# Optimization experiments

Hardware: AMD Instinct MI355X
Metric: run time of the kernel (lower is better)

The kernel has to match this reference:

```python
import jax, jax.numpy as jnp
import numpy as np

E = 16        # n_routed_experts
K = 2         # n_activated_experts (top-k)
DIM = 1024    # model dim
INTER = 704   # moe_inter_dim
B, S = 4, 1024


def setup_inputs() -> dict:
    key = jax.random.key(0)
    ks = jax.random.split(key, 5)
    x = jax.random.normal(ks[0], (B, S, DIM), dtype=jnp.float32)
    Wg = jax.random.normal(ks[1], (E, DIM), dtype=jnp.float32) * 0.02   # gate (Linear, no bias)
    W1 = jax.random.normal(ks[2], (E, DIM, INTER), dtype=jnp.float32) * 0.02
    W3 = jax.random.normal(ks[3], (E, DIM, INTER), dtype=jnp.float32) * 0.02
    W2 = jax.random.normal(ks[4], (E, INTER, DIM), dtype=jnp.float32) * 0.02
    return {"x": x, "Wg": Wg, "W1": W1, "W2": W2, "W3": W3}


def reference(x, Wg, W1, W2, W3):
    # Single-process semantics of MoEWithAll2All: the all2all dispatch/combine is
    # pure communication; the math is: softmax router -> top-k -> renormalize ->
    # per-expert SwiGLU MLP on routed tokens -> weighted combine at original slots.
    Bb, Ss, D = x.shape
    xf = x.reshape(-1, D)                              # [N, D], N = B*S
    logits = xf @ Wg.T                                 # [N, E]
    probs = jax.nn.softmax(logits, axis=-1)
    topw, topi = jax.lax.top_k(probs, K)               # [N, K]
    topw = topw / topw.sum(axis=-1, keepdims=True)
    # gates[n, e] = routed weight of token n for expert e (0 if not routed):
    # identical math to the masked gather/scatter dispatch in the original.
    gates = (jax.nn.one_hot(topi, E, dtype=xf.dtype) * topw[..., None]).sum(axis=1)  # [N, E]
    out = jnp.zeros_like(xf)
    for e in range(E):                                 # small fixed loop over experts
        h = jax.nn.silu(xf @ W1[e]) * (xf @ W3[e])     # SwiGLU expert, [N, INTER]
        out = out + gates[:, e:e + 1] * (h @ W2[e])    # combine with gate weights
    return out.reshape(Bb, Ss, D)
```

## Files before the change

### kernel.cpp

```cpp
#include <hip/hip_runtime.h>

#define NTOK 4096
#define DDIM 1024
#define IDIM 704
#define NEXP 16
#define NSLOT 8192
#define MAXT 128
#define NPAD1 768

typedef __attribute__((ext_vector_type(8))) short bf16x8;
typedef __attribute__((ext_vector_type(4))) float f32x4;
typedef __attribute__((ext_vector_type(4))) unsigned short us4;
typedef __attribute__((ext_vector_type(8))) unsigned short us8;

__device__ __forceinline__ unsigned short f2bf(float f) {
  union { float f; unsigned int u; } v; v.f = f;
  unsigned int r = v.u + 0x7fffu + ((v.u >> 16) & 1u);
  return (unsigned short)(r >> 16);
}

__device__ __forceinline__ void gload_lds16(const void* g, void* l) {
  __builtin_amdgcn_global_load_lds((const __attribute__((address_space(1))) void*)g,
                                   (__attribute__((address_space(3))) void*)l, 16, 0, 0);
}

__global__ void k_router(const float* __restrict__ x, const float* __restrict__ Wg,
                         int* __restrict__ tok_e, float* __restrict__ tok_w,
                         unsigned short* __restrict__ Xb) {
  int lane = threadIdx.x & 63;
  int wv = threadIdx.x >> 6;
  int t = blockIdx.x * 4 + wv;
  const f32x4* xr = (const f32x4*)(x + (size_t)t * DDIM);
  us4* xbr = (us4*)(Xb + (size_t)t * DDIM);
  f32x4 xv[4];
#pragma unroll
  for (int c = 0; c < 4; ++c) {
    xv[c] = xr[c * 64 + lane];
    us4 o;
#pragma unroll
    for (int j = 0; j < 4; ++j) o[j] = f2bf(xv[c][j]);
    xbr[c * 64 + lane] = o;
  }
  float p[NEXP];
#pragma unroll
  for (int e = 0; e < NEXP; ++e) {
    const f32x4* wr = (const f32x4*)(Wg + (size_t)e * DDIM);
    float s = 0.f;
#pragma unroll
    for (int c = 0; c < 4; ++c) {
      f32x4 w4 = wr[c * 64 + lane];
      s += xv[c][0]*w4[0] + xv[c][1]*w4[1] + xv[c][2]*w4[2] + xv[c][3]*w4[3];
    }
    p[e] = s;
  }
#pragma unroll
  for (int off = 32; off >= 1; off >>= 1) {
#pragma unroll
    for (int e = 0; e < NEXP; ++e) p[e] += __shfl_xor(p[e], off);
  }
  int i0 = 0; float b0 = p[0];
#pragma unroll
  for (int e = 1; e < NEXP; ++e) if (p[e] > b0) { b0 = p[e]; i0 = e; }
  int i1 = -1; float b1 = -3.4e38f;
#pragma unroll
  for (int e = 0; e < NEXP; ++e) if (e != i0 && p[e] > b1) { b1 = p[e]; i1 = e; }
  if (lane == 0) {
    float w0 = 1.f / (1.f + __expf(b1 - b0));
    tok_e[2*t] = i0; tok_e[2*t+1] = i1;
    tok_w[2*t] = w0; tok_w[2*t+1] = 1.f - w0;
  }
}

__global__ void k_wtrans(const float* __restrict__ src, unsigned short* __restrict__ dst,
                         int ksz, int nsz, int npad) {
  int e = blockIdx.z;
  int k0 = blockIdx.x * 64, n0 = blockIdx.y * 64;
  src += (size_t)e * ksz * nsz;
  dst += (size_t)e * npad * ksz;
  int t = threadIdx.x;
  if (n0 >= nsz) {
    int nr = t >> 3, kc0 = (t & 7) * 8;
    us8 z = (us8)(unsigned short)0;
#pragma unroll
    for (int p = 0; p < 2; ++p)
      *(us8*)(dst + (size_t)(n0 + nr + p * 32) * ksz + k0 + kc0) = z;
    return;
  }
  __shared__ unsigned short lds[64 * 64];
  int kr4 = (t >> 4) * 4, nc4 = (t & 15) * 4;
  f32x4 v[4];
#pragma unroll
  for (int j = 0; j < 4; ++j)
    v[j] = *(const f32x4*)(src + (size_t)(k0 + kr4 + j) * nsz + n0 + nc4);
  int c8 = kr4 >> 3, half = (kr4 >> 2) & 1;
#pragma unroll
  for (int i = 0; i < 4; ++i) {
    us4 o;
#pragma unroll
    for (int j = 0; j < 4; ++j) o[j] = f2bf(v[j][i]);
    int row = nc4 + i;
    int addr = row * 64 + ((c8 ^ ((row >> 2) & 7)) << 3) + half * 4;
    *(us4*)(lds + addr) = o;
  }
  __syncthreads();
  int nr = t >> 3, kc8 = t & 7;
#pragma unroll
  for (int p = 0; p < 2; ++p) {
    int row = nr + p * 32;
    us8 o = *(const us8*)(lds + row * 64 + ((kc8 ^ ((row >> 2) & 7)) << 3));
    *(us8*)(dst + (size_t)(n0 + row) * ksz + k0 + kc8 * 8) = o;
  }
}

__global__ void k_count_scan(const int* __restrict__ tok_e, int* __restrict__ counts,
                             int* __restrict__ offsets, int* __restrict__ ntiles,
                             int* __restrict__ tile_e, int* __restrict__ tile_m0) {
  __shared__ int h[256 * 17];
  __shared__ int counts_s[NEXP];
  int t = threadIdx.x;
  int c[NEXP];
#pragma unroll
  for (int e = 0; e < NEXP; ++e) c[e] = 0;
  for (int i = t; i < NSLOT; i += 256) {
    int te = tok_e[i];
#pragma unroll
    for (int e = 0; e < NEXP; ++e) c[e] += (te == e) ? 1 : 0;
  }
#pragma unroll
  for (int e = 0; e < NEXP; ++e) h[t * 17 + e] = c[e];
  __syncthreads();
  if (t < NEXP) {
    int s = 0;
    for (int i = 0; i < 256; ++i) s += h[i * 17 + t];
    counts_s[t] = s;
    counts[t] = s;
  }
  __syncthreads();
  if (t == 0) {
    int acc = 0, nt = 0;
    for (int e = 0; e < NEXP; ++e) {
      offsets[e] = acc;
      int cc = counts_s[e];
      for (int m0 = 0; m0 < cc; m0 += 128) { tile_e[nt] = e; tile_m0[nt] = m0; ++nt; }
      acc += cc;
    }
    offsets[NEXP] = acc;
    *ntiles = nt;
  }
}

__global__ void k_scatter2(const int* __restrict__ tok_e, const float* __restrict__ tok_w,
                           const int* __restrict__ offsets, int* __restrict__ token_map,
                           float* __restrict__ gate_w, int* __restrict__ slot_of) {
  int e = blockIdx.x;
  int t = threadIdx.x, lane = t & 63, wv = t >> 6;
  int te[32]; float tw[32];
#pragma unroll
  for (int c = 0; c < 32; ++c) {
    te[c] = tok_e[c * 256 + t];
    tw[c] = tok_w[c * 256 + t];
  }
  __shared__ int wsum[4];
  int run = offsets[e];
  unsigned long long below = (lane == 63) ? 0x7fffffffffffffffull : ((1ull << lane) - 1ull);
#pragma unroll 1
  for (int c = 0; c < 32; ++c) {
    bool f = (te[c] == e);
    unsigned long long m = __ballot(f);
    if (lane == 0) wsum[wv] = __popcll(m);
    __syncthreads();
    int base = run;
    for (int w = 0; w < wv; ++w) base += wsum[w];
    int tot = wsum[0] + wsum[1] + wsum[2] + wsum[3];
    if (f) {
      int i = c * 256 + t;
      int slot = base + __popcll(m & below);
      token_map[slot] = i >> 1;
      gate_w[slot] = tw[c];
      slot_of[i] = slot;
    }
    run += tot;
    __syncthreads();
  }
}

__global__ __launch_bounds__(256, 2)
void k_gemm1(const unsigned short* __restrict__ Xb, const unsigned short* __restrict__ W1T,
             const unsigned short* __restrict__ W3T, const int* __restrict__ token_map,
             const float* __restrict__ gate_w, const int* __restrict__ ntiles,
             const int* __restrict__ tile_e, const int* __restrict__ tile_m0,
             const int* __restrict__ offsets, const int* __restrict__ counts,
             unsigned short* __restrict__ H) {
  int idx = blockIdx.x;
  int xcd = idx & 7, r = idx >> 3;
  int g = (r >> 2) * 8 + xcd;
  int mm = r & 3;
  int ty = (g / 6) * 4 + mm;
  if (ty >= *ntiles) return;
  int n0 = (g % 6) * 128;
  int e = tile_e[ty], m0 = tile_m0[ty];
  int base_slot = offsets[e] + m0;
  int cnt = counts[e] - m0; if (cnt > 128) cnt = 128;

  __shared__ unsigned short As[128 * 32];
  __shared__ unsigned short B1s[128 * 32];
  __shared__ unsigned short B3s[128 * 32];

  int t = threadIdx.x;
  int row = t >> 2, kc = (t & 3) * 8;
  int r0i = base_slot + row;      if (r0i > NSLOT - 1) r0i = NSLOT - 1;
  int r1i = base_slot + 64 + row; if (r1i > NSLOT - 1) r1i = NSLOT - 1;
  const unsigned short* ag0 = Xb + (size_t)token_map[r0i] * DDIM + kc;
  const unsigned short* ag1 = Xb + (size_t)token_map[r1i] * DDIM + kc;
  const unsigned short* b1g0 = W1T + ((size_t)e * NPAD1 + n0 + row) * DDIM + kc;
  const unsigned short* b1g1 = b1g0 + (size_t)64 * DDIM;
  const unsigned short* b3g0 = W3T + ((size_t)e * NPAD1 + n0 + row) * DDIM + kc;
  const unsigned short* b3g1 = b3g0 + (size_t)64 * DDIM;
  unsigned short* asd0 = As + t * 8;   unsigned short* asd1 = As + 2048 + t * 8;
  unsigned short* b1d0 = B1s + t * 8;  unsigned short* b1d1 = B1s + 2048 + t * 8;
  unsigned short* b3d0 = B3s + t * 8;  unsigned short* b3d1 = B3s + 2048 + t * 8;

  int lane = t & 63, wv = t >> 6;
  int wm = (wv >> 1) * 64, wn = (wv & 1) * 64;
  int lm = lane & 15, kg = lane >> 4;
  int ao[4], bo[4];
#pragma unroll
  for (int i = 0; i < 4; ++i) {
    ao[i] = (wm + i * 16 + lm) * 32 + kg * 8;
    bo[i] = (wn + i * 16 + lm) * 32 + kg * 8;
  }

  f32x4 acc1[4][4], acc3[4][4];
#pragma unroll
  for (int i = 0; i < 4; ++i)
#pragma unroll
    for (int j = 0; j < 4; ++j) { acc1[i][j] = 0.f; acc3[i][j] = 0.f; }

  for (int k0 = 0; k0 < DDIM; k0 += 32) {
    __syncthreads();
    gload_lds16(ag0 + k0, asd0);
    gload_lds16(ag1 + k0, asd1);
    gload_lds16(b1g0 + k0, b1d0);
    gload_lds16(b1g1 + k0, b1d1);
    gload_lds16(b3g0 + k0, b3d0);
    gload_lds16(b3g1 + k0, b3d1);
    __syncthreads();
    bf16x8 av[4], b1v[4], b3v[4];
#pragma unroll
    for (int i = 0; i < 4; ++i) {
      av[i]  = *(const bf16x8*)(As + ao[i]);
      b1v[i] = *(const bf16x8*)(B1s + bo[i]);
      b3v[i] = *(const bf16x8*)(B3s + bo[i]);
    }
#pragma unroll
    for (int mi = 0; mi < 4; ++mi)
#pragma unroll
      for (int ni = 0; ni < 4; ++ni) {
        acc1[mi][ni] = __builtin_amdgcn_mfma_f32_16x16x32_bf16(av[mi], b1v[ni], acc1[mi][ni], 0, 0, 0);
        acc3[mi][ni] = __builtin_amdgcn_mfma_f32_16x16x32_bf16(av[mi], b3v[ni], acc3[mi][ni], 0, 0, 0);
      }
  }

#pragma unroll
  for (int mi = 0; mi < 4; ++mi)
#pragma unroll
    for (int rr = 0; rr < 4; ++rr) {
      int orow = wm + mi * 16 + kg * 4 + rr;
      if (orow < cnt) {
        int slot = base_slot + orow;
        float gw = gate_w[slot];
        unsigned short* hrow = H + (size_t)slot * IDIM;
#pragma unroll
        for (int ni = 0; ni < 4; ++ni) {
          int nn = n0 + wn + ni * 16 + lm;
          if (nn < IDIM) {
            float v1 = acc1[mi][ni][rr];
            float v3 = acc3[mi][ni][rr];
            float h = v1 / (1.f + __expf(-v1)) * v3 * gw;
            hrow[nn] = f2bf(h);
          }
        }
      }
    }
}

__global__ __launch_bounds__(256, 3)
void k_gemm2(const unsigned short* __restrict__ H, const unsigned short* __restrict__ W2T,
             const int* __restrict__ ntiles, const int* __restrict__ tile_e,
             const int* __restrict__ tile_m0, const int* __restrict__ offsets,
             const int* __restrict__ counts, float* __restrict__ O2) {
  int idx = blockIdx.x;
  int xcd = idx & 7, r = idx >> 3;
  int g = (r >> 2) * 8 + xcd;
  int mm = r & 3;
  int ty = (g >> 3) * 4 + mm;
  if (ty >= *ntiles) return;
  int n0 = (g & 7) * 128;
  int e = tile_e[ty], m0 = tile_m0[ty];
  int base_slot = offsets[e] + m0;
  int cnt = counts[e] - m0; if (cnt > 128) cnt = 128;

  __shared__ unsigned short As[128 * 32];
  __shared__ unsigned short Bs[128 * 32];

  int t = threadIdx.x;
  int row = t >> 2, kc = (t & 3) * 8;
  int r0i = base_slot + row;      if (r0i > NSLOT - 1) r0i = NSLOT - 1;
  int r1i = base_slot + 64 + row; if (r1i > NSLOT - 1) r1i = NSLOT - 1;
  const unsigned short* ag0 = H + (size_t)r0i * IDIM + kc;
  const unsigned short* ag1 = H + (size_t)r1i * IDIM + kc;
  const unsigned short* bg0 = W2T + ((size_t)e * DDIM + n0 + row) * IDIM + kc;
  const unsigned short* bg1 = bg0 + (size_t)64 * IDIM;
  unsigned short* asd0 = As + t * 8;  unsigned short* asd1 = As + 2048 + t * 8;
  unsigned short* bd0 = Bs + t * 8;   unsigned short* bd1 = Bs + 2048 + t * 8;

  int lane = t & 63, wv = t >> 6;
  int wm = (wv >> 1) * 64, wn = (wv & 1) * 64;
  int lm = lane & 15, kg = lane >> 4;
  int ao[4], bo[4];
#pragma unroll
  for (int i = 0; i < 4; ++i) {
    ao[i] = (wm + i * 16 + lm) * 32 + kg * 8;
    bo[i] = (wn + i * 16 + lm) * 32 + kg * 8;
  }

  f32x4 acc[4][4];
#pragma unroll
  for (int i = 0; i < 4; ++i)
#pragma unroll
    for (int j = 0; j < 4; ++j) acc[i][j] = 0.f;

  for (int k0 = 0; k0 < IDIM; k0 += 32) {
    __syncthreads();
    gload_lds16(ag0 + k0, asd0);
    gload_lds16(ag1 + k0, asd1);
    gload_lds16(bg0 + k0, bd0);
    gload_lds16(bg1 + k0, bd1);
    __syncthreads();
    bf16x8 av[4], bv[4];
#pragma unroll
    for (int i = 0; i < 4; ++i) {
      av[i] = *(const bf16x8*)(As + ao[i]);
      bv[i] = *(const bf16x8*)(Bs + bo[i]);
    }
#pragma unroll
    for (int mi = 0; mi < 4; ++mi)
#pragma unroll
      for (int ni = 0; ni < 4; ++ni)
        acc[mi][ni] = __builtin_amdgcn_mfma_f32_16x16x32_bf16(av[mi], bv[ni], acc[mi][ni], 0, 0, 0);
  }

#pragma unroll
  for (int mi = 0; mi < 4; ++mi)
#pragma unroll
    for (int rr = 0; rr < 4; ++rr) {
      int orow = wm + mi * 16 + kg * 4 + rr;
      if (orow < cnt) {
        float* op = O2 + (size_t)(base_slot + orow) * DDIM + n0;
#pragma unroll
        for (int ni = 0; ni < 4; ++ni)
          op[wn + ni * 16 + lm] = acc[mi][ni][rr];
      }
    }
}

__global__ void k_combine(const float* __restrict__ O2, const int* __restrict__ slot_of,
                          float* __restrict__ out) {
  int tk = blockIdx.x, tt = threadIdx.x;
  int s0 = slot_of[2 * tk], s1 = slot_of[2 * tk + 1];
  f32x4 a = ((const f32x4*)(O2 + (size_t)s0 * DDIM))[tt];
  f32x4 b = ((const f32x4*)(O2 + (size_t)s1 * DDIM))[tt];
  ((f32x4*)(out + (size_t)tk * DDIM))[tt] = a + b;
}

extern "C" void kernel_launch(void* const* d_in, const int* in_sizes, int n_in,
                              void* d_out, int out_size, void* d_ws, size_t ws_size,
                              hipStream_t stream) {
  const float* x  = (const float*)d_in[0];
  const float* Wg = (const float*)d_in[1];
  const float* W1 = (const float*)d_in[2];
  const float* W2 = (const float*)d_in[3];
  const float* W3 = (const float*)d_in[4];
  float* out = (float*)d_out;

  char* ws = (char*)d_ws;
  size_t off = 0;
  unsigned short* Xb = (unsigned short*)(ws + off); off += (size_t)NTOK * DDIM * 2;
  unsigned short* H  = (unsigned short*)(ws + off); off += (size_t)NSLOT * IDIM * 2;
  float* O2 = (float*)(ws + off); off += (size_t)NSLOT * DDIM * 4;
  unsigned short* W1T = (unsigned short*)(ws + off); off += (size_t)NEXP * NPAD1 * DDIM * 2;
  unsigned short* W3T = (unsigned short*)(ws + off); off += (size_t)NEXP * NPAD1 * DDIM * 2;
  unsigned short* W2T = (unsigned short*)(ws + off); off += (size_t)NEXP * DDIM * IDIM * 2;
  int* counts  = (int*)(ws + off); off += 64;
  int* offsets = (int*)(ws + off); off += 128;
  int* ntiles  = (int*)(ws + off); off += 64;
  int* tile_e  = (int*)(ws + off); off += MAXT * 4;
  int* tile_m0 = (int*)(ws + off); off += MAXT * 4;
  int* tok_e   = (int*)(ws + off); off += NSLOT * 4;
  float* tok_w = (float*)(ws + off); off += NSLOT * 4;
  int* token_map = (int*)(ws + off); off += NSLOT * 4;
  float* gate_w  = (float*)(ws + off); off += NSLOT * 4;
  int* slot_of   = (int*)(ws + off); off += NSLOT * 4;

  k_router<<<1024, 256, 0, stream>>>(x, Wg, tok_e, tok_w, Xb);
  k_count_scan<<<1, 256, 0, stream>>>(tok_e, counts, offsets, ntiles, tile_e, tile_m0);
  k_scatter2<<<NEXP, 256, 0, stream>>>(tok_e, tok_w, offsets, token_map, gate_w, slot_of);
  k_wtrans<<<dim3(16, 12, NEXP), 256, 0, stream>>>(W1, W1T, DDIM, IDIM, NPAD1);
  k_wtrans<<<dim3(16, 12, NEXP), 256, 0, stream>>>(W3, W3T, DDIM, IDIM, NPAD1);
  k_gemm1<<<480, 256, 0, stream>>>(Xb, W1T, W3T, token_map, gate_w, ntiles, tile_e,
                                   tile_m0, offsets, counts, H);
  k_wtrans<<<dim3(11, 16, NEXP), 256, 0, stream>>>(W2, W2T, IDIM, DDIM, DDIM);
  k_gemm2<<<640, 256, 0, stream>>>(H, W2T, ntiles, tile_e, tile_m0, offsets, counts, O2);
  k_combine<<<4096, 256, 0, stream>>>(O2, slot_of, out);
}
```

Measured before the change: 308.1 us.

## Halve GEMM M-tile to 64 rows and merge weight transposes into one launch

Both grouped expert GEMMs now use 64-row token tiles instead of 128. Each of the four waves covers all 64 rows and a 32-column slice, so accumulators per thread shrink and launch bounds rise for more occupancy. The tile count and grid sizes double, which cuts padding waste on partial expert tiles. The three weight-transpose launches are folded into a single kernel indexed by flat block id. The trade-off is less A/B reuse per block and more total weight traffic from smaller M tiles.

```diff
diff --git a/kernel.cpp b/kernel.cpp
--- a/kernel.cpp
+++ b/kernel.cpp
@@ -5,7 +5,7 @@
 #define IDIM 704
 #define NEXP 16
 #define NSLOT 8192
-#define MAXT 128
+#define MAXT 160
 #define NPAD1 768
 
 typedef __attribute__((ext_vector_type(8))) short bf16x8;
@@ -71,10 +71,25 @@
   }
 }
 
-__global__ void k_wtrans(const float* __restrict__ src, unsigned short* __restrict__ dst,
-                         int ksz, int nsz, int npad) {
-  int e = blockIdx.z;
-  int k0 = blockIdx.x * 64, n0 = blockIdx.y * 64;
+__global__ void k_wtrans_all(const float* __restrict__ W1, const float* __restrict__ W3,
+                             const float* __restrict__ W2, unsigned short* __restrict__ W1T,
+                             unsigned short* __restrict__ W3T, unsigned short* __restrict__ W2T) {
+  int b = blockIdx.x;
+  const float* src; unsigned short* dst;
+  int ksz, nsz, npad, kx, ny, e;
+  if (b < 6144) {
+    int which = (b >= 3072) ? 1 : 0;
+    int tb = b - which * 3072;
+    kx = tb & 15; int rest = tb >> 4; ny = rest % 12; e = rest / 12;
+    ksz = DDIM; nsz = IDIM; npad = NPAD1;
+    src = which ? W3 : W1; dst = which ? W3T : W1T;
+  } else {
+    int tb = b - 6144;
+    kx = tb % 11; int rest = tb / 11; ny = rest & 15; e = rest >> 4;
+    ksz = IDIM; nsz = DDIM; npad = DDIM;
+    src = W2; dst = W2T;
+  }
+  int k0 = kx * 64, n0 = ny * 64;
   src += (size_t)e * ksz * nsz;
   dst += (size_t)e * npad * ksz;
   int t = threadIdx.x;
@@ -141,7 +156,7 @@
     for (int e = 0; e < NEXP; ++e) {
       offsets[e] = acc;
       int cc = counts_s[e];
-      for (int m0 = 0; m0 < cc; m0 += 128) { tile_e[nt] = e; tile_m0[nt] = m0; ++nt; }
+      for (int m0 = 0; m0 < cc; m0 += 64) { tile_e[nt] = e; tile_m0[nt] = m0; ++nt; }
       acc += cc;
     }
     offsets[NEXP] = acc;
@@ -184,7 +199,7 @@
   }
 }
 
-__global__ __launch_bounds__(256, 2)
+__global__ __launch_bounds__(256, 3)
 void k_gemm1(const unsigned short* __restrict__ Xb, const unsigned short* __restrict__ W1T,
              const unsigned short* __restrict__ W3T, const int* __restrict__ token_map,
              const float* __restrict__ gate_w, const int* __restrict__ ntiles,
@@ -193,69 +208,65 @@
              unsigned short* __restrict__ H) {
   int idx = blockIdx.x;
   int xcd = idx & 7, r = idx >> 3;
-  int g = (r >> 2) * 8 + xcd;
-  int mm = r & 3;
-  int ty = (g / 6) * 4 + mm;
+  int g = (r >> 3) * 8 + xcd;
+  int mm = r & 7;
+  int ty = (g / 6) * 8 + mm;
   if (ty >= *ntiles) return;
   int n0 = (g % 6) * 128;
   int e = tile_e[ty], m0 = tile_m0[ty];
   int base_slot = offsets[e] + m0;
-  int cnt = counts[e] - m0; if (cnt > 128) cnt = 128;
-
-  __shared__ unsigned short As[128 * 32];
+  int cnt = counts[e] - m0; if (cnt > 64) cnt = 64;
+
+  __shared__ unsigned short As[64 * 32];
   __shared__ unsigned short B1s[128 * 32];
   __shared__ unsigned short B3s[128 * 32];
 
   int t = threadIdx.x;
-  int row = t >> 2, kc = (t & 3) * 8;
-  int r0i = base_slot + row;      if (r0i > NSLOT - 1) r0i = NSLOT - 1;
-  int r1i = base_slot + 64 + row; if (r1i > NSLOT - 1) r1i = NSLOT - 1;
+  int rs = t >> 2, kc = (t & 3) * 8;
+  int r0i = base_slot + rs; if (r0i > NSLOT - 1) r0i = NSLOT - 1;
   const unsigned short* ag0 = Xb + (size_t)token_map[r0i] * DDIM + kc;
-  const unsigned short* ag1 = Xb + (size_t)token_map[r1i] * DDIM + kc;
-  const unsigned short* b1g0 = W1T + ((size_t)e * NPAD1 + n0 + row) * DDIM + kc;
+  const unsigned short* b1g0 = W1T + ((size_t)e * NPAD1 + n0 + rs) * DDIM + kc;
   const unsigned short* b1g1 = b1g0 + (size_t)64 * DDIM;
-  const unsigned short* b3g0 = W3T + ((size_t)e * NPAD1 + n0 + row) * DDIM + kc;
+  const unsigned short* b3g0 = W3T + ((size_t)e * NPAD1 + n0 + rs) * DDIM + kc;
   const unsigned short* b3g1 = b3g0 + (size_t)64 * DDIM;
-  unsigned short* asd0 = As + t * 8;   unsigned short* asd1 = As + 2048 + t * 8;
+  unsigned short* asd  = As + t * 8;
   unsigned short* b1d0 = B1s + t * 8;  unsigned short* b1d1 = B1s + 2048 + t * 8;
   unsigned short* b3d0 = B3s + t * 8;  unsigned short* b3d1 = B3s + 2048 + t * 8;
 
   int lane = t & 63, wv = t >> 6;
-  int wm = (wv >> 1) * 64, wn = (wv & 1) * 64;
   int lm = lane & 15, kg = lane >> 4;
-  int ao[4], bo[4];
-#pragma unroll
-  for (int i = 0; i < 4; ++i) {
-    ao[i] = (wm + i * 16 + lm) * 32 + kg * 8;
-    bo[i] = (wn + i * 16 + lm) * 32 + kg * 8;
-  }
-
-  f32x4 acc1[4][4], acc3[4][4];
+  int ao[4], bo[2];
+#pragma unroll
+  for (int i = 0; i < 4; ++i) ao[i] = (i * 16 + lm) * 32 + kg * 8;
+#pragma unroll
+  for (int i = 0; i < 2; ++i) bo[i] = (wv * 32 + i * 16 + lm) * 32 + kg * 8;
+
+  f32x4 acc1[4][2], acc3[4][2];
 #pragma unroll
   for (int i = 0; i < 4; ++i)
 #pragma unroll
-    for (int j = 0; j < 4; ++j) { acc1[i][j] = 0.f; acc3[i][j] = 0.f; }
+    for (int j = 0; j < 2; ++j) { acc1[i][j] = 0.f; acc3[i][j] = 0.f; }
 
   for (int k0 = 0; k0 < DDIM; k0 += 32) {
     __syncthreads();
-    gload_lds16(ag0 + k0, asd0);
-    gload_lds16(ag1 + k0, asd1);
+    gload_lds16(ag0 + k0, asd);
     gload_lds16(b1g0 + k0, b1d0);
     gload_lds16(b1g1 + k0, b1d1);
     gload_lds16(b3g0 + k0, b3d0);
     gload_lds16(b3g1 + k0, b3d1);
     __syncthreads();
-    bf16x8 av[4], b1v[4], b3v[4];
-#pragma unroll
-    for (int i = 0; i < 4; ++i) {
-      av[i]  = *(const bf16x8*)(As + ao[i]);
+    bf16x8 av[4], b1v[2], b3v[2];
+#pragma unroll
+    for (int i = 0; i < 4; ++i) av[i] = *(const bf16x8*)(As + ao[i]);
+#pragma unroll
+    for (int i = 0; i < 2; ++i) {
       b1v[i] = *(const bf16x8*)(B1s + bo[i]);
       b3v[i] = *(const bf16x8*)(B3s + bo[i]);
     }
 #pragma unroll
     for (int mi = 0; mi < 4; ++mi)
 #pragma unroll
-      for (int ni = 0; ni < 4; ++ni) {
+      for (int ni = 0; ni < 2; ++ni) {
         acc1[mi][ni] = __builtin_amdgcn_mfma_f32_16x16x32_bf16(av[mi], b1v[ni], acc1[mi][ni], 0, 0, 0);
         acc3[mi][ni] = __builtin_amdgcn_mfma_f32_16x16x32_bf16(av[mi], b3v[ni], acc3[mi][ni], 0, 0, 0);
       }
@@ -265,14 +276,14 @@
   for (int mi = 0; mi < 4; ++mi)
 #pragma unroll
     for (int rr = 0; rr < 4; ++rr) {
-      int orow = wm + mi * 16 + kg * 4 + rr;
+      int orow = mi * 16 + kg * 4 + rr;
       if (orow < cnt) {
         int slot = base_slot + orow;
         float gw = gate_w[slot];
         unsigned short* hrow = H + (size_t)slot * IDIM;
 #pragma unroll
-        for (int ni = 0; ni < 4; ++ni) {
-          int nn = n0 + wn + ni * 16 + lm;
+        for (int ni = 0; ni < 2; ++ni) {
+          int nn = n0 + wv * 32 + ni * 16 + lm;
           if (nn < IDIM) {
             float v1 = acc1[mi][ni][rr];
             float v3 = acc3[mi][ni][rr];
@@ -284,69 +295,63 @@
     }
 }
 
-__global__ __launch_bounds__(256, 3)
+__global__ __launch_bounds__(256, 4)
 void k_gemm2(const unsigned short* __restrict__ H, const unsigned short* __restrict__ W2T,
              const int* __restrict__ ntiles, const int* __restrict__ tile_e,
              const int* __restrict__ tile_m0, const int* __restrict__ offsets,
              const int* __restrict__ counts, float* __restrict__ O2) {
   int idx = blockIdx.x;
   int xcd = idx & 7, r = idx >> 3;
-  int g = (r >> 2) * 8 + xcd;
-  int mm = r & 3;
-  int ty = (g >> 3) * 4 + mm;
+  int g = (r >> 3) * 8 + xcd;
+  int mm = r & 7;
+  int ty = (g >> 3) * 8 + mm;
   if (ty >= *ntiles) return;
   int n0 = (g & 7) * 128;
   int e = tile_e[ty], m0 = tile_m0[ty];
   int base_slot = offsets[e] + m0;
-  int cnt = counts[e] - m0; if (cnt > 128) cnt = 128;
-
-  __shared__ unsigned short As[128 * 32];
+  int cnt = counts[e] - m0; if (cnt > 64) cnt = 64;
+
+  __shared__ unsigned short As[64 * 32];
   __shared__ unsigned short Bs[128 * 32];
 
   int t = threadIdx.x;
-  int row = t >> 2, kc = (t & 3) * 8;
-  int r0i = base_slot + row;      if (r0i > NSLOT - 1) r0i = NSLOT - 1;
-  int r1i = base_slot + 64 + row; if (r1i > NSLOT - 1) r1i = NSLOT - 1;
+  int rs = t >> 2, kc = (t & 3) * 8;
+  int r0i = base_slot + rs; if (r0i > NSLOT - 1) r0i = NSLOT - 1;
   const unsigned short* ag0 = H + (size_t)r0i * IDIM + kc;
-  const unsigned short* ag1 = H + (size_t)r1i * IDIM + kc;
-  const unsigned short* bg0 = W2T + ((size_t)e * DDIM + n0 + row) * IDIM + kc;
+  const unsigned short* bg0 = W2T + ((size_t)e * DDIM + n0 + rs) * IDIM + kc;
   const unsigned short* bg1 = bg0 + (size_t)64 * IDIM;
-  unsigned short* asd0 = As + t * 8;  unsigned short* asd1 = As + 2048 + t * 8;
-  unsigned short* bd0 = Bs + t * 8;   unsigned short* bd1 = Bs + 2048 + t * 8;
+  unsigned short* asd = As + t * 8;
+  unsigned short* bd0 = Bs + t * 8;  unsigned short* bd1 = Bs + 2048 + t * 8;
 
   int lane = t & 63, wv = t >> 6;
-  int wm = (wv >> 1) * 64, wn = (wv & 1) * 64;
   int lm = lane & 15, kg = lane >> 4;
-  int ao[4], bo[4];
-#pragma unroll
-  for (int i = 0; i < 4; ++i) {
-    ao[i] = (wm + i * 16 + lm) * 32 + kg * 8;
-    bo[i] = (wn + i * 16 + lm) * 32 + kg * 8;
-  }
-
-  f32x4 acc[4][4];
+  int ao[4], bo[2];
+#pragma unroll
+  for (int i = 0; i < 4; ++i) ao[i] = (i * 16 + lm) * 32 + kg * 8;
+#pragma unroll
+  for (int i = 0; i < 2; ++i) bo[i] = (wv * 32 + i * 16 + lm) * 32 + kg * 8;
+
+  f32x4 acc[4][2];
 #pragma unroll
   for (int i = 0; i < 4; ++i)
 #pragma unroll
-    for (int j = 0; j < 4; ++j) acc[i][j] = 0.f;
+    for (int j = 0; j < 2; ++j) acc[i][j] = 0.f;
 
   for (int k0 = 0; k0 < IDIM; k0 += 32) {
     __syncthreads();
-    gload_lds16(ag0 + k0, asd0);
-    gload_lds16(ag1 + k0, asd1);
+    gload_lds16(ag0 + k0, asd);
     gload_lds16(bg0 + k0, bd0);
     gload_lds16(bg1 + k0, bd1);
     __syncthreads();
-    bf16x8 av[4], bv[4];
-#pragma unroll
-    for (int i = 0; i < 4; ++i) {
-      av[i] = *(const bf16x8*)(As + ao[i]);
-      bv[i] = *(const bf16x8*)(Bs + bo[i]);
-    }
+    bf16x8 av[4], bv[2];
+#pragma unroll
+    for (int i = 0; i < 4; ++i) av[i] = *(const bf16x8*)(As + ao[i]);
+#pragma unroll
+    for (int i = 0; i < 2; ++i) bv[i] = *(const bf16x8*)(Bs + bo[i]);
 #pragma unroll
     for (int mi = 0; mi < 4; ++mi)
 #pragma unroll
-      for (int ni = 0; ni < 4; ++ni)
+      for (int ni = 0; ni < 2; ++ni)
         acc[mi][ni] = __builtin_amdgcn_mfma_f32_16x16x32_bf16(av[mi], bv[ni], acc[mi][ni], 0, 0, 0);
   }
 
@@ -354,12 +359,12 @@
   for (int mi = 0; mi < 4; ++mi)
 #pragma unroll
     for (int rr = 0; rr < 4; ++rr) {
-      int orow = wm + mi * 16 + kg * 4 + rr;
+      int orow = mi * 16 + kg * 4 + rr;
       if (orow < cnt) {
         float* op = O2 + (size_t)(base_slot + orow) * DDIM + n0;
 #pragma unroll
-        for (int ni = 0; ni < 4; ++ni)
-          op[wn + ni * 16 + lm] = acc[mi][ni][rr];
+        for (int ni = 0; ni < 2; ++ni)
+          op[wv * 32 + ni * 16 + lm] = acc[mi][ni][rr];
       }
     }
 }
@@ -405,11 +410,9 @@
   k_router<<<1024, 256, 0, stream>>>(x, Wg, tok_e, tok_w, Xb);
   k_count_scan<<<1, 256, 0, stream>>>(tok_e, counts, offsets, ntiles, tile_e, tile_m0);
   k_scatter2<<<NEXP, 256, 0, stream>>>(tok_e, tok_w, offsets, token_map, gate_w, slot_of);
-  k_wtrans<<<dim3(16, 12, NEXP), 256, 0, stream>>>(W1, W1T, DDIM, IDIM, NPAD1);
-  k_wtrans<<<dim3(16, 12, NEXP), 256, 0, stream>>>(W3, W3T, DDIM, IDIM, NPAD1);
-  k_gemm1<<<480, 256, 0, stream>>>(Xb, W1T, W3T, token_map, gate_w, ntiles, tile_e,
+  k_wtrans_all<<<8960, 256, 0, stream>>>(W1, W3, W2, W1T, W3T, W2T);
+  k_gemm1<<<960, 256, 0, stream>>>(Xb, W1T, W3T, token_map, gate_w, ntiles, tile_e,
                                    tile_m0, offsets, counts, H);
-  k_wtrans<<<dim3(11, 16, NEXP), 256, 0, stream>>>(W2, W2T, IDIM, DDIM, DDIM);
-  k_gemm2<<<640, 256, 0, stream>>>(H, W2T, ntiles, tile_e, tile_m0, offsets, counts, O2);
+  k_gemm2<<<1280, 256, 0, stream>>>(H, W2T, ntiles, tile_e, tile_m0, offsets, counts, O2);
   k_combine<<<4096, 256, 0, stream>>>(O2, slot_of, out);
 }
```

After: 319.6 us. 1.04x slower.

## Double-buffer GEMM LDS loads and fuse scan/scatter and weight-transpose launches

Applied to the files above, without the earlier changes.

Both expert GEMMs now use two LDS buffers, so the global-to-LDS loads for the next K-slice are issued while MFMAs run on the current slice, and the second barrier per iteration is dropped. The count/scan and scatter kernels merge into one 16-block kernel in which every block recomputes the expert histogram. The three weight-transpose launches merge into a single launch where each block handles two 64-wide tiles. This trades more LDS per block (which may limit occupancy) and redundant histogram work for less load latency and fewer kernel launches.

```diff
diff --git a/kernel.cpp b/kernel.cpp
--- a/kernel.cpp
+++ b/kernel.cpp
@@ -71,60 +71,29 @@
   }
 }
 
-__global__ void k_wtrans(const float* __restrict__ src, unsigned short* __restrict__ dst,
-                         int ksz, int nsz, int npad) {
-  int e = blockIdx.z;
-  int k0 = blockIdx.x * 64, n0 = blockIdx.y * 64;
-  src += (size_t)e * ksz * nsz;
-  dst += (size_t)e * npad * ksz;
-  int t = threadIdx.x;
-  if (n0 >= nsz) {
-    int nr = t >> 3, kc0 = (t & 7) * 8;
-    us8 z = (us8)(unsigned short)0;
-#pragma unroll
-    for (int p = 0; p < 2; ++p)
-      *(us8*)(dst + (size_t)(n0 + nr + p * 32) * ksz + k0 + kc0) = z;
-    return;
-  }
-  __shared__ unsigned short lds[64 * 64];
-  int kr4 = (t >> 4) * 4, nc4 = (t & 15) * 4;
-  f32x4 v[4];
-#pragma unroll
-  for (int j = 0; j < 4; ++j)
-    v[j] = *(const f32x4*)(src + (size_t)(k0 + kr4 + j) * nsz + n0 + nc4);
-  int c8 = kr4 >> 3, half = (kr4 >> 2) & 1;
-#pragma unroll
-  for (int i = 0; i < 4; ++i) {
-    us4 o;
-#pragma unroll
-    for (int j = 0; j < 4; ++j) o[j] = f2bf(v[j][i]);
-    int row = nc4 + i;
-    int addr = row * 64 + ((c8 ^ ((row >> 2) & 7)) << 3) + half * 4;
-    *(us4*)(lds + addr) = o;
-  }
-  __syncthreads();
-  int nr = t >> 3, kc8 = t & 7;
-#pragma unroll
-  for (int p = 0; p < 2; ++p) {
-    int row = nr + p * 32;
-    us8 o = *(const us8*)(lds + row * 64 + ((kc8 ^ ((row >> 2) & 7)) << 3));
-    *(us8*)(dst + (size_t)(n0 + row) * ksz + k0 + kc8 * 8) = o;
-  }
-}
-
-__global__ void k_count_scan(const int* __restrict__ tok_e, int* __restrict__ counts,
-                             int* __restrict__ offsets, int* __restrict__ ntiles,
-                             int* __restrict__ tile_e, int* __restrict__ tile_m0) {
+__global__ void k_scan_scatter(const int* __restrict__ tok_e, const float* __restrict__ tok_w,
+                               int* __restrict__ counts, int* __restrict__ offsets,
+                               int* __restrict__ ntiles, int* __restrict__ tile_e,
+                               int* __restrict__ tile_m0, int* __restrict__ token_map,
+                               float* __restrict__ gate_w, int* __restrict__ slot_of) {
+  int eb = blockIdx.x;
+  int t = threadIdx.x, lane = t & 63, wv = t >> 6;
   __shared__ int h[256 * 17];
   __shared__ int counts_s[NEXP];
-  int t = threadIdx.x;
+  __shared__ int wsum[4];
+  int te[32]; float tw[32];
+#pragma unroll
+  for (int c = 0; c < 32; ++c) {
+    te[c] = tok_e[c * 256 + t];
+    tw[c] = tok_w[c * 256 + t];
+  }
   int c[NEXP];
 #pragma unroll
   for (int e = 0; e < NEXP; ++e) c[e] = 0;
-  for (int i = t; i < NSLOT; i += 256) {
-    int te = tok_e[i];
-#pragma unroll
-    for (int e = 0; e < NEXP; ++e) c[e] += (te == e) ? 1 : 0;
+#pragma unroll
+  for (int i = 0; i < 32; ++i) {
+#pragma unroll
+    for (int e = 0; e < NEXP; ++e) c[e] += (te[i] == e) ? 1 : 0;
   }
 #pragma unroll
   for (int e = 0; e < NEXP; ++e) h[t * 17 + e] = c[e];
@@ -133,10 +102,13 @@
     int s = 0;
     for (int i = 0; i < 256; ++i) s += h[i * 17 + t];
     counts_s[t] = s;
-    counts[t] = s;
+    if (eb == 0) counts[t] = s;
   }
   __syncthreads();
-  if (t == 0) {
+  int off_e = 0;
+#pragma unroll
+  for (int e = 0; e < NEXP; ++e) off_e += (e < eb) ? counts_s[e] : 0;
+  if (eb == 0 && t == 0) {
     int acc = 0, nt = 0;
     for (int e = 0; e < NEXP; ++e) {
       offsets[e] = acc;
@@ -147,25 +119,11 @@
     offsets[NEXP] = acc;
     *ntiles = nt;
   }
-}
-
-__global__ void k_scatter2(const int* __restrict__ tok_e, const float* __restrict__ tok_w,
-                           const int* __restrict__ offsets, int* __restrict__ token_map,
-                           float* __restrict__ gate_w, int* __restrict__ slot_of) {
-  int e = blockIdx.x;
-  int t = threadIdx.x, lane = t & 63, wv = t >> 6;
-  int te[32]; float tw[32];
-#pragma unroll
-  for (int c = 0; c < 32; ++c) {
-    te[c] = tok_e[c * 256 + t];
-    tw[c] = tok_w[c * 256 + t];
-  }
-  __shared__ int wsum[4];
-  int run = offsets[e];
+  int run = off_e;
   unsigned long long below = (lane == 63) ? 0x7fffffffffffffffull : ((1ull << lane) - 1ull);
 #pragma unroll 1
-  for (int c = 0; c < 32; ++c) {
-    bool f = (te[c] == e);
+  for (int cc = 0; cc < 32; ++cc) {
+    bool f = (te[cc] == eb);
     unsigned long long m = __ballot(f);
     if (lane == 0) wsum[wv] = __popcll(m);
     __syncthreads();
@@ -173,14 +131,75 @@
     for (int w = 0; w < wv; ++w) base += wsum[w];
     int tot = wsum[0] + wsum[1] + wsum[2] + wsum[3];
     if (f) {
-      int i = c * 256 + t;
+      int i = cc * 256 + t;
       int slot = base + __popcll(m & below);
       token_map[slot] = i >> 1;
-      gate_w[slot] = tw[c];
+      gate_w[slot] = tw[cc];
       slot_of[i] = slot;
     }
     run += tot;
     __syncthreads();
+  }
+}
+
+__global__ void k_wtrans_all(const float* __restrict__ W1, const float* __restrict__ W3,
+                             const float* __restrict__ W2, unsigned short* __restrict__ W1T,
+                             unsigned short* __restrict__ W3T, unsigned short* __restrict__ W2T) {
+  int b = blockIdx.x;
+  const float* src; unsigned short* dst;
+  int ksz, nsz, kx, np, e;
+  if (b < 3072) {
+    int which = (b >= 1536) ? 1 : 0;
+    int tb = b - which * 1536;
+    kx = tb & 15; int rest = tb >> 4; np = rest % 6; e = rest / 6;
+    ksz = DDIM; nsz = IDIM;
+    src = (which ? W3 : W1) + (size_t)e * DDIM * IDIM;
+    dst = (which ? W3T : W1T) + (size_t)e * NPAD1 * DDIM;
+  } else {
+    int tb = b - 3072;
+    kx = tb % 11; int rest = tb / 11; np = rest & 7; e = rest >> 3;
+    ksz = IDIM; nsz = DDIM;
+    src = W2 + (size_t)e * IDIM * DDIM;
+    dst = W2T + (size_t)e * DDIM * IDIM;
+  }
+  int k0 = kx * 64;
+  __shared__ unsigned short lds[64 * 64];
+  int t = threadIdx.x;
+#pragma unroll
+  for (int p = 0; p < 2; ++p) {
+    int n0 = np * 128 + p * 64;
+    if (p) __syncthreads();
+    if (n0 >= nsz) {
+      int nr = t >> 3, kc0 = (t & 7) * 8;
+      us8 z = (us8)(unsigned short)0;
+#pragma unroll
+      for (int q = 0; q < 2; ++q)
+        *(us8*)(dst + (size_t)(n0 + nr + q * 32) * ksz + k0 + kc0) = z;
+      continue;
+    }
+    int kr4 = (t >> 4) * 4, nc4 = (t & 15) * 4;
+    f32x4 v[4];
+#pragma unroll
+    for (int j = 0; j < 4; ++j)
+      v[j] = *(const f32x4*)(src + (size_t)(k0 + kr4 + j) * nsz + n0 + nc4);
+    int c8 = kr4 >> 3, half = (kr4 >> 2) & 1;
+#pragma unroll
+    for (int i = 0; i < 4; ++i) {
+      us4 o;
+#pragma unroll
+      for (int j = 0; j < 4; ++j) o[j] = f2bf(v[j][i]);
+      int row = nc4 + i;
+      int addr = row * 64 + ((c8 ^ ((row >> 2) & 7)) << 3) + half * 4;
+      *(us4*)(lds + addr) = o;
+    }
+    __syncthreads();
+    int nr = t >> 3, kc8 = t & 7;
+#pragma unroll
+    for (int q = 0; q < 2; ++q) {
+      int row = nr + q * 32;
+      us8 o = *(const us8*)(lds + row * 64 + ((kc8 ^ ((row >> 2) & 7)) << 3));
+      *(us8*)(dst + (size_t)(n0 + row) * ksz + k0 + kc8 * 8) = o;
+    }
   }
 }
 
@@ -202,9 +221,9 @@
   int base_slot = offsets[e] + m0;
   int cnt = counts[e] - m0; if (cnt > 128) cnt = 128;
 
-  __shared__ unsigned short As[128 * 32];
-  __shared__ unsigned short B1s[128 * 32];
-  __shared__ unsigned short B3s[128 * 32];
+  __shared__ unsigned short As[2][128 * 32];
+  __shared__ unsigned short B1s[2][128 * 32];
+  __shared__ unsigned short B3s[2][128 * 32];
 
   int t = threadIdx.x;
   int row = t >> 2, kc = (t & 3) * 8;
@@ -216,9 +235,7 @@
   const unsigned short* b1g1 = b1g0 + (size_t)64 * DDIM;
   const unsigned short* b3g0 = W3T + ((size_t)e * NPAD1 + n0 + row) * DDIM + kc;
   const unsigned short* b3g1 = b3g0 + (size_t)64 * DDIM;
-  unsigned short* asd0 = As + t * 8;   unsigned short* asd1 = As + 2048 + t * 8;
-  unsigned short* b1d0 = B1s + t * 8;  unsigned short* b1d1 = B1s + 2048 + t * 8;
-  unsigned short* b3d0 = B3s + t * 8;  unsigned short* b3d1 = B3s + 2048 + t * 8;
+  int d0 = t * 8, d1 = 2048 + t * 8;
 
   int lane = t & 63, wv = t >> 6;
   int wm = (wv >> 1) * 64, wn = (wv & 1) * 64;
@@ -236,21 +253,31 @@
 #pragma unroll
     for (int j = 0; j < 4; ++j) { acc1[i][j] = 0.f; acc3[i][j] = 0.f; }
 
+  gload_lds16(ag0, As[0] + d0);
+  gload_lds16(ag1, As[0] + d1);
+  gload_lds16(b1g0, B1s[0] + d0);
+  gload_lds16(b1g1, B1s[0] + d1);
+  gload_lds16(b3g0, B3s[0] + d0);
+  gload_lds16(b3g1, B3s[0] + d1);
+
   for (int k0 = 0; k0 < DDIM; k0 += 32) {
+    int cur = (k0 >> 5) & 1;
     __syncthreads();
-    gload_lds16(ag0 + k0, asd0);
-    gload_lds16(ag1 + k0, asd1);
-    gload_lds16(b1g0 + k0, b1d0);
-    gload_lds16(b1g1 + k0, b1d1);
-    gload_lds16(b3g0 + k0, b3d0);
-    gload_lds16(b3g1 + k0, b3d1);
-    __syncthreads();
+    if (k0 + 32 < DDIM) {
+      int nx = cur ^ 1, kn = k0 + 32;
+      gload_lds16(ag0 + kn, As[nx] + d0);
+      gload_lds16(ag1 + kn, As[nx] + d1);
+      gload_lds16(b1g0 + kn, B1s[nx] + d0);
+      gload_lds16(b1g1 + kn, B1s[nx] + d1);
+      gload_lds16(b3g0 + kn, B3s[nx] + d0);
+      gload_lds16(b3g1 + kn, B3s[nx] + d1);
+    }
     bf16x8 av[4], b1v[4], b3v[4];
 #pragma unroll
     for (int i = 0; i < 4; ++i) {
-      av[i]  = *(const bf16x8*)(As + ao[i]);
-      b1v[i] = *(const bf16x8*)(B1s + bo[i]);
-      b3v[i] = *(const bf16x8*)(B3s + bo[i]);
+      av[i]  = *(const bf16x8*)(As[cur] + ao[i]);
+      b1v[i] = *(const bf16x8*)(B1s[cur] + bo[i]);
+      b3v[i] = *(const bf16x8*)(B3s[cur] + bo[i]);
     }
 #pragma unroll
     for (int mi = 0; mi < 4; ++mi)
@@ -300,8 +327,8 @@
   int base_slot = offsets[e] + m0;
   int cnt = counts[e] - m0; if (cnt > 128) cnt = 128;
 
-  __shared__ unsigned short As[128 * 32];
-  __shared__ unsigned short Bs[128 * 32];
+  __shared__ unsigned short As[2][128 * 32];
+  __shared__ unsigned short Bs[2][128 * 32];
 
   int t = threadIdx.x;
   int row = t >> 2, kc = (t & 3) * 8;
@@ -311,8 +338,7 @@
   const unsigned short* ag1 = H + (size_t)r1i * IDIM + kc;
   const unsigned short* bg0 = W2T + ((size_t)e * DDIM + n0 + row) * IDIM + kc;
   const unsigned short* bg1 = bg0 + (size_t)64 * IDIM;
-  unsigned short* asd0 = As + t * 8;  unsigned short* asd1 = As + 2048 + t * 8;
-  unsigned short* bd0 = Bs + t * 8;   unsigned short* bd1 = Bs + 2048 + t * 8;
+  int d0 = t * 8, d1 = 2048 + t * 8;
 
   int lane = t & 63, wv = t >> 6;
   int wm = (wv >> 1) * 64, wn = (wv & 1) * 64;
@@ -330,18 +356,26 @@
 #pragma unroll
     for (int j = 0; j < 4; ++j) acc[i][j] = 0.f;
 
+  gload_lds16(ag0, As[0] + d0);
+  gload_lds16(ag1, As[0] + d1);
+  gload_lds16(bg0, Bs[0] + d0);
+  gload_lds16(bg1, Bs[0] + d1);
+
   for (int k0 = 0; k0 < IDIM; k0 += 32) {
+    int cur = (k0 >> 5) & 1;
     __syncthreads();
-    gload_lds16(ag0 + k0, asd0);
-    gload_lds16(ag1 + k0, asd1);
-    gload_lds16(bg0 + k0, bd0);
-    gload_lds16(bg1 + k0, bd1);
-    __syncthreads();
+    if (k0 + 32 < IDIM) {
+      int nx = cur ^ 1, kn = k0 + 32;
+      gload_lds16(ag0 + kn, As[nx] + d0);
+      gload_lds16(ag1 + kn, As[nx] + d1);
+      gload_lds16(bg0 + kn, Bs[nx] + d0);
+      gload_lds16(bg1 + kn, Bs[nx] + d1);
+    }
     bf16x8 av[4], bv[4];
 #pragma unroll
     for (int i = 0; i < 4; ++i) {
-      av[i] = *(const bf16x8*)(As + ao[i]);
-      bv[i] = *(const bf16x8*)(Bs + bo[i]);
+      av[i] = *(const bf16x8*)(As[cur] + ao[i]);
+      bv[i] = *(const bf16x8*)(Bs[cur] + bo[i]);
     }
 #pragma unroll
     for (int mi = 0; mi < 4; ++mi)
@@ -403,13 +437,11 @@
   int* slot_of   = (int*)(ws + off); off += NSLOT * 4;
 
   k_router<<<1024, 256, 0, stream>>>(x, Wg, tok_e, tok_w, Xb);
-  k_count_scan<<<1, 256, 0, stream>>>(tok_e, counts, offsets, ntiles, tile_e, tile_m0);
-  k_scatter2<<<NEXP, 256, 0, stream>>>(tok_e, tok_w, offsets, token_map, gate_w, slot_of);
-  k_wtrans<<<dim3(16, 12, NEXP), 256, 0, stream>>>(W1, W1T, DDIM, IDIM, NPAD1);
-  k_wtrans<<<dim3(16, 12, NEXP), 256, 0, stream>>>(W3, W3T, DDIM, IDIM, NPAD1);
+  k_scan_scatter<<<NEXP, 256, 0, stream>>>(tok_e, tok_w, counts, offsets, ntiles,
+                                           tile_e, tile_m0, token_map, gate_w, slot_of);
+  k_wtrans_all<<<4480, 256, 0, stream>>>(W1, W3, W2, W1T, W3T, W2T);
   k_gemm1<<<480, 256, 0, stream>>>(Xb, W1T, W3T, token_map, gate_w, ntiles, tile_e,
                                    tile_m0, offsets, counts, H);
-  k_wtrans<<<dim3(11, 16, NEXP), 256, 0, stream>>>(W2, W2T, IDIM, DDIM, DDIM);
   k_gemm2<<<640, 256, 0, stream>>>(H, W2T, ntiles, tile_e, tile_m0, offsets, counts, O2);
   k_combine<<<4096, 256, 0, stream>>>(O2, slot_of, out);
 }
```

New measurement: 312.1 us. No clear change (+1.3%).
